# Kernel tuning notes

Measured on AMD Instinct MI355X. Metric: run time of the kernel, lower is better.

## Reference

```python
import jax, jax.numpy as jnp
import numpy as np

DT = 0.001          # continuous-dynamics step (dt > 0 branch)
KERNEL_SIZE = 16384 # L
P, H = 1024, 256    # d_state, d_input (= d_output)


def setup_inputs() -> dict:
    key = jax.random.key(0)
    kAr, kAi, kB, kC = jax.random.split(key, 4)
    # Continuous diagonal state matrix: real part in [strong, weak] = [-0.5, -0.01] (stable),
    # imaginary part uniform in [-pi, pi] (mimics diagonal_state_space_matrix init).
    Ar = jax.random.uniform(kAr, (P,), minval=-0.5, maxval=-0.01)
    Ai = jax.random.uniform(kAi, (P,), minval=-np.pi, maxval=np.pi)
    A = jnp.stack([Ar, Ai], axis=-1).astype(jnp.float32)            # (P, 2) view_as_real
    # B, C ~ uniform disk (radius 1): scaled complex gaussians are a fine stand-in numerically.
    B = (jax.random.normal(kB, (P, H, 2)) / np.sqrt(H)).astype(jnp.float32)   # (P, H, 2)
    C = (jax.random.normal(kC, (H, P, 2)) / np.sqrt(P)).astype(jnp.float32)   # (H, P, 2)
    return {"A": A, "B": B, "C": C}


def _as_complex(x):
    return x[..., 0] + 1j * x[..., 1]


def reference(A, B, C):
    """Vandermonde SSM kernel generation (continuous dt > 0 branch).
    Returns kernel (H, L, 2) = real view of complex kernel (H, L)."""
    Ac = _as_complex(A)   # (P,) complex
    Bc = _as_complex(B)   # (P, H)
    Cc = _as_complex(C)   # (H, P)

    # ZOH-style discretization
    A_bar = jnp.exp(Ac * DT)                               # (P,)
    B_bar = ((A_bar - 1.0) / Ac)[:, None] * Bc             # (P, H)

    # Vandermonde matrix V[p, l] = A_bar[p] ** l  (complex power == exp(l * log(a)))
    powers = jnp.arange(KERNEL_SIZE, dtype=jnp.float32)    # (L,)
    V = jnp.exp(jnp.log(A_bar)[:, None] * powers[None, :]) # (P, L)

    # W[h, p] = C[h, p] * B_bar[p, h]; kernel[h, l] = sum_p W[h, p] * V[p, l]
    W = Cc * B_bar.T                                       # (H, P)
    kernel = jnp.einsum('hp,pl->hl', W, V)                 # (H, L) complex
    return jnp.stack([kernel.real, kernel.imag], axis=-1)  # (H, L, 2) float32
```

## Files before the change

### kernel.cpp

```cpp
#include <hip/hip_runtime.h>
#include <hip/hip_fp16.h>

#define P_DIM 1024
#define H_DIM 256
#define L_DIM 16384
#define DT 0.001f
#define TWOPI 6.283185307179586f
#define INV2PI 0.15915494309189535f
#define WSCALE 4096.0f
#define INV_WSCALE (1.0f / 4096.0f)
#define BM 128
#define BN 128
#define BK 64
#define NT 256
#define LDB 72

typedef _Float16 f16x8 __attribute__((ext_vector_type(8)));
typedef float f32x4 __attribute__((ext_vector_type(4)));

#define GPTR(p) (const __attribute__((address_space(1))) unsigned*)(p)
#define LPTR(p) (__attribute__((address_space(3))) unsigned*)(p)

union H2U { __half2 h; unsigned u; };

__device__ __forceinline__ float2 cmulf(float2 a, float2 b) {
    return make_float2(a.x * b.x - a.y * b.y, a.x * b.y + a.y * b.x);
}

__global__ __launch_bounds__(256)
void prep_kernel(const float* __restrict__ Ag, const float* __restrict__ Bg,
                 const float* __restrict__ Cg, __half* __restrict__ W2) {
    __shared__ float2 Bt[64][33];
    __shared__ float2 sc[64];
    const int t  = threadIdx.x;
    const int p0 = (blockIdx.x & 15) << 6;
    const int h0 = (blockIdx.x >> 4) << 5;

    if (t < 64) {
        float2 a = ((const float2*)Ag)[p0 + t];
        float er = __expf(a.x * DT);
        float s, c; __sincosf(a.y * DT, &s, &c);
        float nr = er * c - 1.f, ni = er * s;
        float inv = 1.f / (a.x * a.x + a.y * a.y);
        sc[t] = make_float2((nr * a.x + ni * a.y) * inv, (ni * a.x - nr * a.y) * inv);
    }
    #pragma unroll
    for (int i = 0; i < 8; ++i) {
        int idx = i * 256 + t, p = idx >> 5, h = idx & 31;
        Bt[p][h] = ((const float2*)Bg)[(size_t)(p0 + p) * H_DIM + h0 + h];
    }
    __syncthreads();
    #pragma unroll
    for (int i = 0; i < 8; ++i) {
        int idx = i * 256 + t, h = idx >> 6, p = idx & 63;
        float2 cc = ((const float2*)Cg)[(size_t)(h0 + h) * P_DIM + p0 + p];
        float2 s2 = sc[p], b = Bt[p][h];
        float2 tv = cmulf(cc, s2);
        float wr = (tv.x * b.x - tv.y * b.y) * WSCALE;
        float wi = (tv.x * b.y + tv.y * b.x) * WSCALE;
        ((__half2*)W2)[(size_t)(h0 + h) * P_DIM + p0 + p] =
            __float22half2_rn(make_float2(wr, wi));
    }
}

__global__ __launch_bounds__(NT, 2)
void vand_mfma_kernel(const float* __restrict__ Ag,
                      const _Float16* __restrict__ W2,
                      float* __restrict__ out) {
    __shared__ __attribute__((aligned(16))) _Float16 As[2][BM * BK];
    __shared__ __attribute__((aligned(16))) _Float16 Bs[2][BN * LDB];
    __shared__ float2 Atab[P_DIM];

    const int tid  = threadIdx.x;
    const int lane = tid & 63;
    const int w    = tid >> 6;
    const int wm   = w & 1, wn = w >> 1;
    const int m0   = blockIdx.y * BM;
    const int nb   = blockIdx.x * BN;
    const int lb   = blockIdx.x * (BN / 2);

    const float2* Ag2 = (const float2*)Ag;

    #pragma unroll
    for (int i = 0; i < 4; ++i) {
        int p = tid + i * 256;
        float2 a = Ag2[p];
        float e = __expf(a.x * DT);
        float s, c; __sincosf(a.y * DT, &s, &c);
        Atab[p] = make_float2(e * c, e * s);
    }

    f32x4 acc[4][4];
    #pragma unroll
    for (int mt = 0; mt < 4; ++mt)
        #pragma unroll
        for (int nt = 0; nt < 4; ++nt)
            acc[mt][nt] = (f32x4){0.f, 0.f, 0.f, 0.f};

    const int pl    = tid & 31;
    const int lg    = tid >> 5;
    const float l0f = (float)(lb + lg * 8);
    const int bpbase = lg * 16 * LDB + 2 * pl;

    const int goff = (lane >> 3) * 2048 + (((lane & 7) ^ (lane >> 3)) << 3);
    const _Float16* gwbase = W2 + (size_t)(m0 + (w << 5)) * 2048;
    const int ldsoff = (w << 5) * 64;

    _Float16* Acur = &As[0][0]; _Float16* Bcur = &Bs[0][0];
    _Float16* Anxt = &As[1][0]; _Float16* Bnxt = &Bs[1][0];

#define DMA_CHUNK(K0, DST)                                                        \
    {                                                                             \
        const _Float16* gw = gwbase + (K0) + goff;                                \
        _Float16* lB = (DST) + ldsoff;                                            \
        _Pragma("unroll")                                                         \
        for (int r = 0; r < 4; ++r)                                               \
            __builtin_amdgcn_global_load_lds(GPTR(gw + r * 8 * 2048),             \
                                             LPTR(lB + r * 8 * 64), 16, 0, 0);    \
    }

#define VGEN_CHUNK(K0, DST)                                                       \
    {                                                                             \
        const int pg = ((K0) >> 1) + pl;                                          \
        float2 a  = Ag2[pg];                                                      \
        float2 ab = Atab[pg];                                                     \
        float cx = a.x * DT, cy = a.y * (DT * INV2PI);                            \
        float mg = __expf(cx * l0f);                                              \
        float x  = cy * l0f; x -= rintf(x);                                       \
        float s, c; __sincosf(x * TWOPI, &s, &c);                                 \
        float2 v = make_float2(mg * c, mg * s);                                   \
        _Float16* bp = (DST) + bpbase;                                            \
        _Pragma("unroll")                                                         \
        for (int j = 0; j < 8; ++j) {                                             \
            H2U u0, u1;                                                           \
            u0.h = __float22half2_rn(make_float2(v.x, -v.y));                     \
            u1.h = __float22half2_rn(make_float2(v.y, v.x));                      \
            *(unsigned*)(bp + j * 2 * LDB)       = u0.u;                          \
            *(unsigned*)(bp + j * 2 * LDB + LDB) = u1.u;                          \
            if (j < 7) v = cmulf(v, ab);                                          \
        }                                                                         \
    }

    __syncthreads();
    DMA_CHUNK(0, Acur)
    VGEN_CHUNK(0, Bcur)
    __syncthreads();

    for (int kk = 0; kk < 32; ++kk) {
        if (kk < 31) {
            const int k1 = (kk + 1) * BK;
            DMA_CHUNK(k1, Anxt)
            VGEN_CHUNK(k1, Bnxt)
        }
        #pragma unroll
        for (int ks = 0; ks < 2; ++ks) {
            f16x8 af[4], bf[4];
            const int g = ks * 4 + (lane >> 4);
            #pragma unroll
            for (int t = 0; t < 4; ++t) {
                int m = wm * 64 + t * 16 + (lane & 15);
                af[t] = *(const f16x8*)(Acur + m * 64 + ((g ^ (m & 7)) << 3));
                int n = wn * 64 + t * 16 + (lane & 15);
                bf[t] = *(const f16x8*)(Bcur + n * LDB + (g << 3));
            }
            #pragma unroll
            for (int mt = 0; mt < 4; ++mt)
                #pragma unroll
                for (int nt = 0; nt < 4; ++nt)
                    acc[mt][nt] = __builtin_amdgcn_mfma_f32_16x16x32_f16(
                        af[mt], bf[nt], acc[mt][nt], 0, 0, 0);
        }
        __syncthreads();
        _Float16* tA = Acur; Acur = Anxt; Anxt = tA;
        _Float16* tB = Bcur; Bcur = Bnxt; Bnxt = tB;
    }

    #pragma unroll
    for (int mt = 0; mt < 4; ++mt) {
        #pragma unroll
        for (int nt = 0; nt < 4; ++nt) {
            int h = m0 + wm * 64 + mt * 16 + ((lane >> 4) << 2);
            int n = nb + wn * 64 + nt * 16 + (lane & 15);
            #pragma unroll
            for (int r = 0; r < 4; ++r)
                out[(size_t)(h + r) * 32768 + n] = acc[mt][nt][r] * INV_WSCALE;
        }
    }
#undef DMA_CHUNK
#undef VGEN_CHUNK
}

extern "C" void kernel_launch(void* const* d_in, const int* in_sizes, int n_in,
                              void* d_out, int out_size, void* d_ws, size_t ws_size,
                              hipStream_t stream) {
    const float* A = (const float*)d_in[0];
    const float* B = (const float*)d_in[1];
    const float* C = (const float*)d_in[2];
    float* out = (float*)d_out;
    __half* W2 = (__half*)d_ws;

    prep_kernel<<<dim3(128), dim3(256), 0, stream>>>(A, B, C, W2);
    vand_mfma_kernel<<<dim3(L_DIM * 2 / BN, H_DIM / BM), dim3(NT), 0, stream>>>(
        A, (const _Float16*)W2, out);
}
```

Before: 109.6 us.

## Swizzle Vandermonde LDS tile, cache per-state constants, relax pipeline waits

The padded B tile in LDS is replaced by an XOR-swizzled 64-wide layout, for both the Vandermonde writes and the MFMA fragment reads. The per-state table now also holds the pre-scaled real and imaginary parts of A, which removes a global load from each chunk generation. The __syncthreads calls become explicit s_waitcnt plus s_barrier, with vmcnt(4) so the next chunk's async global-to-LDS load can stay in flight across the barrier. The MFMA phase also runs at raised wave priority. LDS use rises slightly because of the larger table, and correctness now depends on the hand-written wait counts.

```diff
diff --git a/kernel.cpp b/kernel.cpp
--- a/kernel.cpp
+++ b/kernel.cpp
@@ -13,7 +13,6 @@
 #define BN 128
 #define BK 64
 #define NT 256
-#define LDB 72
 
 typedef _Float16 f16x8 __attribute__((ext_vector_type(8)));
 typedef float f32x4 __attribute__((ext_vector_type(4)));
@@ -68,8 +67,8 @@
                       const _Float16* __restrict__ W2,
                       float* __restrict__ out) {
     __shared__ __attribute__((aligned(16))) _Float16 As[2][BM * BK];
-    __shared__ __attribute__((aligned(16))) _Float16 Bs[2][BN * LDB];
-    __shared__ float2 Atab[P_DIM];
+    __shared__ __attribute__((aligned(16))) _Float16 Bs[2][BN * BK];
+    __shared__ float4 Atab[P_DIM];
 
     const int tid  = threadIdx.x;
     const int lane = tid & 63;
@@ -87,7 +86,7 @@
         float2 a = Ag2[p];
         float e = __expf(a.x * DT);
         float s, c; __sincosf(a.y * DT, &s, &c);
-        Atab[p] = make_float2(e * c, e * s);
+        Atab[p] = make_float4(e * c, e * s, a.x * DT, a.y * (DT * INV2PI));
     }
 
     f32x4 acc[4][4];
@@ -100,7 +99,9 @@
     const int pl    = tid & 31;
     const int lg    = tid >> 5;
     const float l0f = (float)(lb + lg * 8);
-    const int bpbase = lg * 16 * LDB + 2 * pl;
+    const int cq3   = (pl >> 2) << 3;
+    const int cs    = (2 * pl) & 7;
+    const int vbase = lg * 1024 + cs;
 
     const int goff = (lane >> 3) * 2048 + (((lane & 7) ^ (lane >> 3)) << 3);
     const _Float16* gwbase = W2 + (size_t)(m0 + (w << 5)) * 2048;
@@ -122,36 +123,43 @@
 #define VGEN_CHUNK(K0, DST)                                                       \
     {                                                                             \
         const int pg = ((K0) >> 1) + pl;                                          \
-        float2 a  = Ag2[pg];                                                      \
-        float2 ab = Atab[pg];                                                     \
-        float cx = a.x * DT, cy = a.y * (DT * INV2PI);                            \
-        float mg = __expf(cx * l0f);                                              \
-        float x  = cy * l0f; x -= rintf(x);                                       \
+        float4 t4 = Atab[pg];                                                     \
+        float mg = __expf(t4.z * l0f);                                            \
+        float x  = t4.w * l0f; x -= rintf(x);                                     \
         float s, c; __sincosf(x * TWOPI, &s, &c);                                 \
-        float2 v = make_float2(mg * c, mg * s);                                   \
-        _Float16* bp = (DST) + bpbase;                                            \
+        float2 v  = make_float2(mg * c, mg * s);                                  \
+        float2 ab = make_float2(t4.x, t4.y);                                      \
         _Pragma("unroll")                                                         \
         for (int j = 0; j < 8; ++j) {                                             \
             H2U u0, u1;                                                           \
             u0.h = __float22half2_rn(make_float2(v.x, -v.y));                     \
             u1.h = __float22half2_rn(make_float2(v.y, v.x));                      \
-            *(unsigned*)(bp + j * 2 * LDB)       = u0.u;                          \
-            *(unsigned*)(bp + j * 2 * LDB + LDB) = u1.u;                          \
+            int e0 = vbase + j * 128 + (cq3 ^ (((2 * j) & 7) << 3));              \
+            int e1 = vbase + j * 128 + 64 + (cq3 ^ (((2 * j + 1) & 7) << 3));     \
+            *(unsigned*)((DST) + e0) = u0.u;                                      \
+            *(unsigned*)((DST) + e1) = u1.u;                                      \
             if (j < 7) v = cmulf(v, ab);                                          \
         }                                                                         \
     }
 
+    DMA_CHUNK(0, Acur)
     __syncthreads();
-    DMA_CHUNK(0, Acur)
     VGEN_CHUNK(0, Bcur)
-    __syncthreads();
 
     for (int kk = 0; kk < 32; ++kk) {
         if (kk < 31) {
             const int k1 = (kk + 1) * BK;
             DMA_CHUNK(k1, Anxt)
             VGEN_CHUNK(k1, Bnxt)
+            asm volatile("s_waitcnt vmcnt(4) lgkmcnt(0)" ::: "memory");
+        } else {
+            asm volatile("s_waitcnt vmcnt(0) lgkmcnt(0)" ::: "memory");
         }
+        __builtin_amdgcn_sched_barrier(0);
+        __builtin_amdgcn_s_barrier();
+        __builtin_amdgcn_sched_barrier(0);
+
+        __builtin_amdgcn_s_setprio(1);
         #pragma unroll
         for (int ks = 0; ks < 2; ++ks) {
             f16x8 af[4], bf[4];
@@ -161,7 +169,7 @@
                 int m = wm * 64 + t * 16 + (lane & 15);
                 af[t] = *(const f16x8*)(Acur + m * 64 + ((g ^ (m & 7)) << 3));
                 int n = wn * 64 + t * 16 + (lane & 15);
-                bf[t] = *(const f16x8*)(Bcur + n * LDB + (g << 3));
+                bf[t] = *(const f16x8*)(Bcur + n * 64 + ((g ^ (n & 7)) << 3));
             }
             #pragma unroll
             for (int mt = 0; mt < 4; ++mt)
@@ -170,7 +178,11 @@
                     acc[mt][nt] = __builtin_amdgcn_mfma_f32_16x16x32_f16(
                         af[mt], bf[nt], acc[mt][nt], 0, 0, 0);
         }
-        __syncthreads();
+        __builtin_amdgcn_s_setprio(0);
+        __builtin_amdgcn_sched_barrier(0);
+        __builtin_amdgcn_s_barrier();
+        __builtin_amdgcn_sched_barrier(0);
+
         _Float16* tA = Acur; Acur = Anxt; Anxt = tA;
         _Float16* tB = Bcur; Bcur = Bnxt; Bnxt = tB;
     }
```

Result: no change. 107.9 us (-1.6%).
